# Optimization experiments

Measured on AMD Instinct MI355X. Metric: run time of the kernel, lower is better.

The kernel has to match this reference:

```python
import math
import jax, jax.numpy as jnp
import numpy as np

B = 8
S = 1024  # equal per-sequence length -> cu_seqlens = arange(B+1)*S
H = 16
D = 64


def setup_inputs() -> dict:
    key = jax.random.key(0)
    kq, kk, kv = jax.random.split(key, 3)
    T = B * S
    q = jax.random.normal(kq, (T, H, D), dtype=jnp.float32)
    k = jax.random.normal(kk, (T, H, D), dtype=jnp.float32)
    v = jax.random.normal(kv, (T, H, D), dtype=jnp.float32)
    cu_seqlens = (jnp.arange(B + 1, dtype=jnp.int32) * S)
    return {"q": q, "k": k, "v": v, "cu_seqlens": cu_seqlens, "max_seqlen": S}


def reference(q, k, v, cu_seqlens, max_seqlen):
    # Non-causal varlen attention over packed sequences.
    # q, k, v: [total_tokens, H, D]; cu_seqlens: [B+1] int32.
    # Sequences here are equal-length, so the packed layout reshapes to [B,S,H,D];
    # a cu_seqlens-derived validity mask keeps the math identical to the varlen kernel.
    T, h, d = q.shape
    b = cu_seqlens.shape[0] - 1
    s = T // b
    scale = 1.0 / math.sqrt(d)

    seq_lens = cu_seqlens[1:] - cu_seqlens[:-1]            # [b]
    valid = jnp.arange(s)[None, :] < seq_lens[:, None]      # [b, s] bool

    qb = q.reshape(b, s, h, d)
    kb = k.reshape(b, s, h, d)
    vb = v.reshape(b, s, h, d)

    scores = jnp.einsum("bqhd,bkhd->bhqk", qb, kb) * scale  # [b,h,s,s]
    neg = jnp.asarray(-1e30, dtype=scores.dtype)
    scores = jnp.where(valid[:, None, None, :], scores, neg)
    p = jax.nn.softmax(scores, axis=-1)
    out = jnp.einsum("bhqk,bkhd->bqhd", p, vb)              # [b,s,h,d]
    out = jnp.where(valid[:, :, None, None], out, 0.0)
    return out.reshape(T, h, d)
```

## Files before the change

### kernel.cpp

```cpp
#include <hip/hip_runtime.h>

#define H_DIM 16
#define D_DIM 64
#define QBLK 256
#define KVBLK 64
#define NTHREADS 512
#define TOKSTRIDE (H_DIM * D_DIM)

typedef __bf16 bf16x8 __attribute__((ext_vector_type(8)));
typedef float  f32x4  __attribute__((ext_vector_type(4)));

__global__ __launch_bounds__(NTHREADS, 4)
void attn_fwd(const float* __restrict__ qg, const float* __restrict__ kg,
              const float* __restrict__ vg, const int* __restrict__ cu,
              float* __restrict__ out, int tiles)
{
    __shared__ __align__(16) __bf16 Klds[2][KVBLK * D_DIM];
    __shared__ __align__(16) __bf16 Vlds[2][KVBLK * D_DIM];

    int nwg = gridDim.x;
    int bid = blockIdx.x;
    int lg = ((nwg & 7) == 0) ? ((bid & 7) * (nwg >> 3) + (bid >> 3)) : bid;

    int qt  = lg % tiles;
    int sh  = lg / tiles;
    int h   = sh % H_DIM;
    int seq = sh / H_DIM;

    int cu0 = cu[seq], cu1 = cu[seq + 1];
    int len = cu1 - cu0;
    int q0  = qt * QBLK;
    if (len <= 0 || q0 >= len) return;

    int tid  = threadIdx.x;
    int wid  = tid >> 6;
    int lane = tid & 63;
    int g    = lane >> 4;
    int c    = lane & 15;

    const float SC = 0.125f * 1.44269504088896340736f;

    bf16x8 qf[2][2];
    #pragma unroll
    for (int rg = 0; rg < 2; ++rg) {
        int qrow = q0 + wid * 32 + rg * 16 + c;
        bool valid = qrow < len;
        const float* qp = qg + ((cu0 + qrow) * TOKSTRIDE + h * D_DIM);
        #pragma unroll
        for (int ks = 0; ks < 2; ++ks) {
            float4 a = valid ? *(const float4*)(qp + ks * 32 + g * 8)     : make_float4(0,0,0,0);
            float4 b = valid ? *(const float4*)(qp + ks * 32 + g * 8 + 4) : make_float4(0,0,0,0);
            qf[rg][ks][0] = (__bf16)(a.x * SC); qf[rg][ks][1] = (__bf16)(a.y * SC);
            qf[rg][ks][2] = (__bf16)(a.z * SC); qf[rg][ks][3] = (__bf16)(a.w * SC);
            qf[rg][ks][4] = (__bf16)(b.x * SC); qf[rg][ks][5] = (__bf16)(b.y * SC);
            qf[rg][ks][6] = (__bf16)(b.z * SC); qf[rg][ks][7] = (__bf16)(b.w * SC);
        }
    }

    f32x4 o0[4] = {}, o1[4] = {};
    float m0 = -3.0e38f, m1 = -3.0e38f;
    float l0 = 0.0f,     l1 = 0.0f;

    int krow = tid >> 3;
    int kc   = tid & 7;
    int kwoff = krow * 128 + ((kc * 16) ^ ((krow & 7) << 4));
    int vfg  = tid >> 6;
    int vd   = tid & 63;
    int vr0  = 32 * (vfg >> 2) + 4 * (vfg & 3);

    const float* kptr = kg + (cu0 + krow) * TOKSTRIDE + h * D_DIM + kc * 8;
    const float* vptr = vg + (cu0 + vr0)  * TOKSTRIDE + h * D_DIM + vd;

    float4 ka, kb;
    float  vv[8];

    auto load_fast = [&]() {
        ka = *(const float4*)kptr;
        kb = *(const float4*)(kptr + 4);
        #pragma unroll
        for (int i = 0; i < 8; ++i)
            vv[i] = vptr[(i >> 2) * (16 * TOKSTRIDE) + (i & 3) * TOKSTRIDE];
        kptr += KVBLK * TOKSTRIDE;
        vptr += KVBLK * TOKSTRIDE;
    };
    auto load_tail = [&](int kb0) {
        if (kb0 + krow < len) {
            ka = *(const float4*)kptr;
            kb = *(const float4*)(kptr + 4);
        } else {
            ka = make_float4(0,0,0,0); kb = make_float4(0,0,0,0);
        }
        #pragma unroll
        for (int i = 0; i < 8; ++i) {
            int r = kb0 + vr0 + 16 * (i >> 2) + (i & 3);
            vv[i] = (r < len) ? vptr[(i >> 2) * (16 * TOKSTRIDE) + (i & 3) * TOKSTRIDE] : 0.f;
        }
        kptr += KVBLK * TOKSTRIDE;
        vptr += KVBLK * TOKSTRIDE;
    };
    auto write_tile = [&](int buf) {
        bf16x8 kw;
        kw[0]=(__bf16)ka.x; kw[1]=(__bf16)ka.y; kw[2]=(__bf16)ka.z; kw[3]=(__bf16)ka.w;
        kw[4]=(__bf16)kb.x; kw[5]=(__bf16)kb.y; kw[6]=(__bf16)kb.z; kw[7]=(__bf16)kb.w;
        *(bf16x8*)((char*)Klds[buf] + kwoff) = kw;
        bf16x8 vw;
        #pragma unroll
        for (int i = 0; i < 8; ++i) vw[i] = (__bf16)vv[i];
        *(bf16x8*)(Vlds[buf] + (tid << 3)) = vw;
    };

    int nkv = (len + KVBLK - 1) / KVBLK;

    if (KVBLK <= len) load_fast(); else load_tail(0);
    write_tile(0);
    __syncthreads();

    int cur = 0;
    for (int kt = 0; kt < nkv; ++kt) {
        int kbase = kt * KVBLK;
        bool more = kt + 1 < nkv;
        if (more) {
            int nb0 = kbase + KVBLK;
            if (nb0 + KVBLK <= len) load_fast(); else load_tail(nb0);
        }

        const __bf16* K = Klds[cur];
        f32x4 s0[4] = {}, s1[4] = {};
        __builtin_amdgcn_s_setprio(1);
        #pragma unroll
        for (int b = 0; b < 4; ++b) {
            int rowk = 16 * b + c;
            int swz = (rowk & 7) << 4;
            const char* base = (const char*)K + rowk * 128;
            bf16x8 a0 = *(const bf16x8*)(base + ((16 * g)      ^ swz));
            bf16x8 a1 = *(const bf16x8*)(base + ((64 + 16 * g) ^ swz));
            s0[b] = __builtin_amdgcn_mfma_f32_16x16x32_bf16(a0, qf[0][0], s0[b], 0, 0, 0);
            s0[b] = __builtin_amdgcn_mfma_f32_16x16x32_bf16(a1, qf[0][1], s0[b], 0, 0, 0);
            s1[b] = __builtin_amdgcn_mfma_f32_16x16x32_bf16(a0, qf[1][0], s1[b], 0, 0, 0);
            s1[b] = __builtin_amdgcn_mfma_f32_16x16x32_bf16(a1, qf[1][1], s1[b], 0, 0, 0);
        }
        __builtin_amdgcn_s_setprio(0);

        if (kbase + KVBLK > len) {
            #pragma unroll
            for (int b = 0; b < 4; ++b)
                #pragma unroll
                for (int r = 0; r < 4; ++r)
                    if (kbase + 16 * b + 4 * g + r >= len) { s0[b][r] = -3.0e38f; s1[b][r] = -3.0e38f; }
        }

        float t0 = fmaxf(fmaxf(fmaxf(s0[0][0],s0[0][1]),fmaxf(s0[0][2],s0[0][3])),
                         fmaxf(fmaxf(s0[1][0],s0[1][1]),fmaxf(s0[1][2],s0[1][3])));
        t0 = fmaxf(t0, fmaxf(fmaxf(fmaxf(s0[2][0],s0[2][1]),fmaxf(s0[2][2],s0[2][3])),
                             fmaxf(fmaxf(s0[3][0],s0[3][1]),fmaxf(s0[3][2],s0[3][3]))));
        float t1 = fmaxf(fmaxf(fmaxf(s1[0][0],s1[0][1]),fmaxf(s1[0][2],s1[0][3])),
                         fmaxf(fmaxf(s1[1][0],s1[1][1]),fmaxf(s1[1][2],s1[1][3])));
        t1 = fmaxf(t1, fmaxf(fmaxf(fmaxf(s1[2][0],s1[2][1]),fmaxf(s1[2][2],s1[2][3])),
                             fmaxf(fmaxf(s1[3][0],s1[3][1]),fmaxf(s1[3][2],s1[3][3]))));
        t0 = fmaxf(t0, __shfl_xor(t0, 16));
        t0 = fmaxf(t0, __shfl_xor(t0, 32));
        t1 = fmaxf(t1, __shfl_xor(t1, 16));
        t1 = fmaxf(t1, __shfl_xor(t1, 32));

        int ok = (t0 <= m0 + 8.f) && (t1 <= m1 + 8.f);
        if (!__all(ok)) {
            float mn0 = fmaxf(m0, t0), mn1 = fmaxf(m1, t1);
            float al0 = __builtin_amdgcn_exp2f(m0 - mn0);
            float al1 = __builtin_amdgcn_exp2f(m1 - mn1);
            m0 = mn0; m1 = mn1; l0 *= al0; l1 *= al1;
            #pragma unroll
            for (int r = 0; r < 4; ++r) {
                float a0f = __shfl(al0, 4 * g + r);
                float a1f = __shfl(al1, 4 * g + r);
                #pragma unroll
                for (int nb = 0; nb < 4; ++nb) { o0[nb][r] *= a0f; o1[nb][r] *= a1f; }
            }
        }

        bf16x8 p0[2], p1[2];
        float ps0 = 0.f, ps1 = 0.f;
        #pragma unroll
        for (int M = 0; M < 2; ++M)
            #pragma unroll
            for (int i = 0; i < 8; ++i) {
                float e0 = __builtin_amdgcn_exp2f(s0[2 * M + (i >> 2)][i & 3] - m0);
                float e1 = __builtin_amdgcn_exp2f(s1[2 * M + (i >> 2)][i & 3] - m1);
                p0[M][i] = (__bf16)e0; p1[M][i] = (__bf16)e1;
                ps0 += e0; ps1 += e1;
            }
        ps0 += __shfl_xor(ps0, 16); ps0 += __shfl_xor(ps0, 32);
        ps1 += __shfl_xor(ps1, 16); ps1 += __shfl_xor(ps1, 32);
        l0 += ps0; l1 += ps1;

        const __bf16* V = Vlds[cur];
        __builtin_amdgcn_s_setprio(1);
        #pragma unroll
        for (int nb = 0; nb < 4; ++nb) {
            #pragma unroll
            for (int M = 0; M < 2; ++M) {
                bf16x8 vf = *(const bf16x8*)(V + ((((M << 2) + g) << 6) + (nb << 4) + c) * 8);
                o0[nb] = __builtin_amdgcn_mfma_f32_16x16x32_bf16(p0[M], vf, o0[nb], 0, 0, 0);
                o1[nb] = __builtin_amdgcn_mfma_f32_16x16x32_bf16(p1[M], vf, o1[nb], 0, 0, 0);
            }
        }
        __builtin_amdgcn_s_setprio(0);

        if (more) write_tile(cur ^ 1);
        __syncthreads();
        cur ^= 1;
    }

    #pragma unroll
    for (int r = 0; r < 4; ++r) {
        float lr0 = __shfl(l0, 4 * g + r);
        float lr1 = __shfl(l1, 4 * g + r);
        float li0 = (lr0 > 0.f) ? 1.0f / lr0 : 0.f;
        float li1 = (lr1 > 0.f) ? 1.0f / lr1 : 0.f;
        int qrowA = q0 + wid * 32 + 4 * g + r;
        int qrowB = qrowA + 16;
        if (qrowA < len) {
            float* op = out + ((cu0 + qrowA) * TOKSTRIDE + h * D_DIM);
            #pragma unroll
            for (int nb = 0; nb < 4; ++nb) op[nb * 16 + c] = o0[nb][r] * li0;
        }
        if (qrowB < len) {
            float* op = out + ((cu0 + qrowB) * TOKSTRIDE + h * D_DIM);
            #pragma unroll
            for (int nb = 0; nb < 4; ++nb) op[nb * 16 + c] = o1[nb][r] * li1;
        }
    }
}

extern "C" void kernel_launch(void* const* d_in, const int* in_sizes, int n_in,
                              void* d_out, int out_size, void* d_ws, size_t ws_size,
                              hipStream_t stream) {
    const float* q  = (const float*)d_in[0];
    const float* k  = (const float*)d_in[1];
    const float* v  = (const float*)d_in[2];
    const int*   cu = (const int*)d_in[3];

    int nseq  = in_sizes[3] - 1;
    int T     = in_sizes[0] / (H_DIM * D_DIM);
    int S     = T / nseq;
    int tiles = (S + QBLK - 1) / QBLK;
    int nwg   = nseq * H_DIM * tiles;

    attn_fwd<<<nwg, NTHREADS, 0, stream>>>(q, k, v, cu, (float*)d_out, tiles);
}
```

Before: 61.26 us.

## Compute softmax row sums via MFMA with ones vector and rotate KV start

Replaces the per-lane exp sum and cross-lane shuffle reduction of the softmax denominator with extra MFMAs that multiply the bf16 probabilities by a ones column, so the row sum accumulates in the matrix unit. Half of the workgroups start their KV loop at the middle tile and wrap around, which spreads KV memory traffic across different addresses at the same moment. The row max now uses three-input max chains. The trade-offs: four extra MFMAs per tile, and a denominator summed from bf16-rounded probabilities rather than fp32 values.

```diff
diff --git a/kernel.cpp b/kernel.cpp
--- a/kernel.cpp
+++ b/kernel.cpp
@@ -9,6 +9,8 @@
 
 typedef __bf16 bf16x8 __attribute__((ext_vector_type(8)));
 typedef float  f32x4  __attribute__((ext_vector_type(4)));
+
+#define MAX3(a,b,c) fmaxf(fmaxf((a),(b)),(c))
 
 __global__ __launch_bounds__(NTHREADS, 4)
 void attn_fwd(const float* __restrict__ qg, const float* __restrict__ kg,
@@ -57,9 +59,13 @@
         }
     }
 
+    bf16x8 ones;
+    #pragma unroll
+    for (int i = 0; i < 8; ++i) ones[i] = (c == 0) ? (__bf16)1.0f : (__bf16)0.0f;
+
     f32x4 o0[4] = {}, o1[4] = {};
+    f32x4 o0x = {}, o1x = {};
     float m0 = -3.0e38f, m1 = -3.0e38f;
-    float l0 = 0.0f,     l1 = 0.0f;
 
     int krow = tid >> 3;
     int kc   = tid & 7;
@@ -68,32 +74,34 @@
     int vd   = tid & 63;
     int vr0  = 32 * (vfg >> 2) + 4 * (vfg & 3);
 
-    const float* kptr = kg + (cu0 + krow) * TOKSTRIDE + h * D_DIM + kc * 8;
-    const float* vptr = vg + (cu0 + vr0)  * TOKSTRIDE + h * D_DIM + vd;
+    const float* kbase_ptr = kg + (cu0 + krow) * TOKSTRIDE + h * D_DIM + kc * 8;
+    const float* vbase_ptr = vg + (cu0 + vr0)  * TOKSTRIDE + h * D_DIM + vd;
+    const float* kptr;
+    const float* vptr;
 
     float4 ka, kb;
     float  vv[8];
 
-    auto load_fast = [&]() {
-        ka = *(const float4*)kptr;
-        kb = *(const float4*)(kptr + 4);
-        #pragma unroll
-        for (int i = 0; i < 8; ++i)
-            vv[i] = vptr[(i >> 2) * (16 * TOKSTRIDE) + (i & 3) * TOKSTRIDE];
-        kptr += KVBLK * TOKSTRIDE;
-        vptr += KVBLK * TOKSTRIDE;
-    };
-    auto load_tail = [&](int kb0) {
-        if (kb0 + krow < len) {
+    auto do_load = [&](int kt) {
+        int kb0 = kt * KVBLK;
+        if (kb0 + KVBLK <= len) {
             ka = *(const float4*)kptr;
             kb = *(const float4*)(kptr + 4);
+            #pragma unroll
+            for (int i = 0; i < 8; ++i)
+                vv[i] = vptr[(i >> 2) * (16 * TOKSTRIDE) + (i & 3) * TOKSTRIDE];
         } else {
-            ka = make_float4(0,0,0,0); kb = make_float4(0,0,0,0);
-        }
-        #pragma unroll
-        for (int i = 0; i < 8; ++i) {
-            int r = kb0 + vr0 + 16 * (i >> 2) + (i & 3);
-            vv[i] = (r < len) ? vptr[(i >> 2) * (16 * TOKSTRIDE) + (i & 3) * TOKSTRIDE] : 0.f;
+            if (kb0 + krow < len) {
+                ka = *(const float4*)kptr;
+                kb = *(const float4*)(kptr + 4);
+            } else {
+                ka = make_float4(0,0,0,0); kb = make_float4(0,0,0,0);
+            }
+            #pragma unroll
+            for (int i = 0; i < 8; ++i) {
+                int r = kb0 + vr0 + 16 * (i >> 2) + (i & 3);
+                vv[i] = (r < len) ? vptr[(i >> 2) * (16 * TOKSTRIDE) + (i & 3) * TOKSTRIDE] : 0.f;
+            }
         }
         kptr += KVBLK * TOKSTRIDE;
         vptr += KVBLK * TOKSTRIDE;
@@ -110,18 +118,23 @@
     };
 
     int nkv = (len + KVBLK - 1) / KVBLK;
-
-    if (KVBLK <= len) load_fast(); else load_tail(0);
+    int kt0 = ((2 * bid >= nwg) && nkv > 1) ? (nkv >> 1) : 0;
+
+    kptr = kbase_ptr + (size_t)kt0 * KVBLK * TOKSTRIDE;
+    vptr = vbase_ptr + (size_t)kt0 * KVBLK * TOKSTRIDE;
+    do_load(kt0);
     write_tile(0);
     __syncthreads();
 
     int cur = 0;
-    for (int kt = 0; kt < nkv; ++kt) {
+    int kt = kt0;
+    for (int ii = 0; ii < nkv; ++ii) {
         int kbase = kt * KVBLK;
-        bool more = kt + 1 < nkv;
+        int ktn = (kt + 1 == nkv) ? 0 : kt + 1;
+        bool more = (ii + 1 < nkv);
         if (more) {
-            int nb0 = kbase + KVBLK;
-            if (nb0 + KVBLK <= len) load_fast(); else load_tail(nb0);
+            if (ktn == 0) { kptr = kbase_ptr; vptr = vbase_ptr; }
+            do_load(ktn);
         }
 
         const __bf16* K = Klds[cur];
@@ -149,14 +162,18 @@
                     if (kbase + 16 * b + 4 * g + r >= len) { s0[b][r] = -3.0e38f; s1[b][r] = -3.0e38f; }
         }
 
-        float t0 = fmaxf(fmaxf(fmaxf(s0[0][0],s0[0][1]),fmaxf(s0[0][2],s0[0][3])),
-                         fmaxf(fmaxf(s0[1][0],s0[1][1]),fmaxf(s0[1][2],s0[1][3])));
-        t0 = fmaxf(t0, fmaxf(fmaxf(fmaxf(s0[2][0],s0[2][1]),fmaxf(s0[2][2],s0[2][3])),
-                             fmaxf(fmaxf(s0[3][0],s0[3][1]),fmaxf(s0[3][2],s0[3][3]))));
-        float t1 = fmaxf(fmaxf(fmaxf(s1[0][0],s1[0][1]),fmaxf(s1[0][2],s1[0][3])),
-                         fmaxf(fmaxf(s1[1][0],s1[1][1]),fmaxf(s1[1][2],s1[1][3])));
-        t1 = fmaxf(t1, fmaxf(fmaxf(fmaxf(s1[2][0],s1[2][1]),fmaxf(s1[2][2],s1[2][3])),
-                             fmaxf(fmaxf(s1[3][0],s1[3][1]),fmaxf(s1[3][2],s1[3][3]))));
+        float x0 = MAX3(s0[0][0], s0[0][1], s0[0][2]);
+        float x1 = MAX3(s0[0][3], s0[1][0], s0[1][1]);
+        float x2 = MAX3(s0[1][2], s0[1][3], s0[2][0]);
+        float x3 = MAX3(s0[2][1], s0[2][2], s0[2][3]);
+        float x4 = MAX3(s0[3][0], s0[3][1], s0[3][2]);
+        float t0 = MAX3(MAX3(x0, x1, x2), fmaxf(x3, x4), s0[3][3]);
+        float y0 = MAX3(s1[0][0], s1[0][1], s1[0][2]);
+        float y1 = MAX3(s1[0][3], s1[1][0], s1[1][1]);
+        float y2 = MAX3(s1[1][2], s1[1][3], s1[2][0]);
+        float y3 = MAX3(s1[2][1], s1[2][2], s1[2][3]);
+        float y4 = MAX3(s1[3][0], s1[3][1], s1[3][2]);
+        float t1 = MAX3(MAX3(y0, y1, y2), fmaxf(y3, y4), s1[3][3]);
         t0 = fmaxf(t0, __shfl_xor(t0, 16));
         t0 = fmaxf(t0, __shfl_xor(t0, 32));
         t1 = fmaxf(t1, __shfl_xor(t1, 16));
@@ -167,30 +184,25 @@
             float mn0 = fmaxf(m0, t0), mn1 = fmaxf(m1, t1);
             float al0 = __builtin_amdgcn_exp2f(m0 - mn0);
             float al1 = __builtin_amdgcn_exp2f(m1 - mn1);
-            m0 = mn0; m1 = mn1; l0 *= al0; l1 *= al1;
+            m0 = mn0; m1 = mn1;
             #pragma unroll
             for (int r = 0; r < 4; ++r) {
                 float a0f = __shfl(al0, 4 * g + r);
                 float a1f = __shfl(al1, 4 * g + r);
                 #pragma unroll
                 for (int nb = 0; nb < 4; ++nb) { o0[nb][r] *= a0f; o1[nb][r] *= a1f; }
+                o0x[r] *= a0f; o1x[r] *= a1f;
             }
         }
 
         bf16x8 p0[2], p1[2];
-        float ps0 = 0.f, ps1 = 0.f;
         #pragma unroll
         for (int M = 0; M < 2; ++M)
             #pragma unroll
             for (int i = 0; i < 8; ++i) {
-                float e0 = __builtin_amdgcn_exp2f(s0[2 * M + (i >> 2)][i & 3] - m0);
-                float e1 = __builtin_amdgcn_exp2f(s1[2 * M + (i >> 2)][i & 3] - m1);
-                p0[M][i] = (__bf16)e0; p1[M][i] = (__bf16)e1;
-                ps0 += e0; ps1 += e1;
-            }
-        ps0 += __shfl_xor(ps0, 16); ps0 += __shfl_xor(ps0, 32);
-        ps1 += __shfl_xor(ps1, 16); ps1 += __shfl_xor(ps1, 32);
-        l0 += ps0; l1 += ps1;
+                p0[M][i] = (__bf16)__builtin_amdgcn_exp2f(s0[2 * M + (i >> 2)][i & 3] - m0);
+                p1[M][i] = (__bf16)__builtin_amdgcn_exp2f(s1[2 * M + (i >> 2)][i & 3] - m1);
+            }
 
         const __bf16* V = Vlds[cur];
         __builtin_amdgcn_s_setprio(1);
@@ -203,17 +215,22 @@
                 o1[nb] = __builtin_amdgcn_mfma_f32_16x16x32_bf16(p1[M], vf, o1[nb], 0, 0, 0);
             }
         }
+        o0x = __builtin_amdgcn_mfma_f32_16x16x32_bf16(p0[0], ones, o0x, 0, 0, 0);
+        o0x = __builtin_amdgcn_mfma_f32_16x16x32_bf16(p0[1], ones, o0x, 0, 0, 0);
+        o1x = __builtin_amdgcn_mfma_f32_16x16x32_bf16(p1[0], ones, o1x, 0, 0, 0);
+        o1x = __builtin_amdgcn_mfma_f32_16x16x32_bf16(p1[1], ones, o1x, 0, 0, 0);
         __builtin_amdgcn_s_setprio(0);
 
         if (more) write_tile(cur ^ 1);
         __syncthreads();
         cur ^= 1;
+        kt = ktn;
     }
 
     #pragma unroll
     for (int r = 0; r < 4; ++r) {
-        float lr0 = __shfl(l0, 4 * g + r);
-        float lr1 = __shfl(l1, 4 * g + r);
+        float lr0 = __shfl(o0x[r], 16 * g);
+        float lr1 = __shfl(o1x[r], 16 * g);
         float li0 = (lr0 > 0.f) ? 1.0f / lr0 : 0.f;
         float li1 = (lr1 > 0.f) ? 1.0f / lr1 : 0.f;
         int qrowA = q0 + wid * 32 + 4 * g + r;
```

New measurement: 82.24 us. 34.2% more time.

## Process two KV tiles per barrier using four-slot LDS ring

Applied to the files above, without the earlier changes.

Grows the K/V LDS buffers from two to four slots and restructures the main loop so each iteration computes two KV tiles before a single __syncthreads, halving the number of block-wide barriers. The load and write logic is merged into one helper and the per-tile compute is factored into a lambda. Doubling LDS to 32 KB per block may limit how many blocks fit per CU under the launch bounds of 4, and it adds register pressure from the duplicated inlined compute.

```diff
diff --git a/kernel.cpp b/kernel.cpp
--- a/kernel.cpp
+++ b/kernel.cpp
@@ -15,8 +15,8 @@
               const float* __restrict__ vg, const int* __restrict__ cu,
               float* __restrict__ out, int tiles)
 {
-    __shared__ __align__(16) __bf16 Klds[2][KVBLK * D_DIM];
-    __shared__ __align__(16) __bf16 Vlds[2][KVBLK * D_DIM];
+    __shared__ __align__(16) __bf16 Klds[4][KVBLK * D_DIM];
+    __shared__ __align__(16) __bf16 Vlds[4][KVBLK * D_DIM];
 
     int nwg = gridDim.x;
     int bid = blockIdx.x;
@@ -74,26 +74,25 @@
     float4 ka, kb;
     float  vv[8];
 
-    auto load_fast = [&]() {
-        ka = *(const float4*)kptr;
-        kb = *(const float4*)(kptr + 4);
-        #pragma unroll
-        for (int i = 0; i < 8; ++i)
-            vv[i] = vptr[(i >> 2) * (16 * TOKSTRIDE) + (i & 3) * TOKSTRIDE];
-        kptr += KVBLK * TOKSTRIDE;
-        vptr += KVBLK * TOKSTRIDE;
-    };
-    auto load_tail = [&](int kb0) {
-        if (kb0 + krow < len) {
+    auto do_load = [&](int kb0) {
+        if (kb0 + KVBLK <= len) {
             ka = *(const float4*)kptr;
             kb = *(const float4*)(kptr + 4);
+            #pragma unroll
+            for (int i = 0; i < 8; ++i)
+                vv[i] = vptr[(i >> 2) * (16 * TOKSTRIDE) + (i & 3) * TOKSTRIDE];
         } else {
-            ka = make_float4(0,0,0,0); kb = make_float4(0,0,0,0);
-        }
-        #pragma unroll
-        for (int i = 0; i < 8; ++i) {
-            int r = kb0 + vr0 + 16 * (i >> 2) + (i & 3);
-            vv[i] = (r < len) ? vptr[(i >> 2) * (16 * TOKSTRIDE) + (i & 3) * TOKSTRIDE] : 0.f;
+            if (kb0 + krow < len) {
+                ka = *(const float4*)kptr;
+                kb = *(const float4*)(kptr + 4);
+            } else {
+                ka = make_float4(0,0,0,0); kb = make_float4(0,0,0,0);
+            }
+            #pragma unroll
+            for (int i = 0; i < 8; ++i) {
+                int r = kb0 + vr0 + 16 * (i >> 2) + (i & 3);
+                vv[i] = (r < len) ? vptr[(i >> 2) * (16 * TOKSTRIDE) + (i & 3) * TOKSTRIDE] : 0.f;
+            }
         }
         kptr += KVBLK * TOKSTRIDE;
         vptr += KVBLK * TOKSTRIDE;
@@ -109,22 +108,8 @@
         *(bf16x8*)(Vlds[buf] + (tid << 3)) = vw;
     };
 
-    int nkv = (len + KVBLK - 1) / KVBLK;
-
-    if (KVBLK <= len) load_fast(); else load_tail(0);
-    write_tile(0);
-    __syncthreads();
-
-    int cur = 0;
-    for (int kt = 0; kt < nkv; ++kt) {
-        int kbase = kt * KVBLK;
-        bool more = kt + 1 < nkv;
-        if (more) {
-            int nb0 = kbase + KVBLK;
-            if (nb0 + KVBLK <= len) load_fast(); else load_tail(nb0);
-        }
-
-        const __bf16* K = Klds[cur];
+    auto compute_tile = [&](int buf, int kbase) {
+        const __bf16* K = Klds[buf];
         f32x4 s0[4] = {}, s1[4] = {};
         __builtin_amdgcn_s_setprio(1);
         #pragma unroll
@@ -149,14 +134,16 @@
                     if (kbase + 16 * b + 4 * g + r >= len) { s0[b][r] = -3.0e38f; s1[b][r] = -3.0e38f; }
         }
 
-        float t0 = fmaxf(fmaxf(fmaxf(s0[0][0],s0[0][1]),fmaxf(s0[0][2],s0[0][3])),
-                         fmaxf(fmaxf(s0[1][0],s0[1][1]),fmaxf(s0[1][2],s0[1][3])));
-        t0 = fmaxf(t0, fmaxf(fmaxf(fmaxf(s0[2][0],s0[2][1]),fmaxf(s0[2][2],s0[2][3])),
-                             fmaxf(fmaxf(s0[3][0],s0[3][1]),fmaxf(s0[3][2],s0[3][3]))));
-        float t1 = fmaxf(fmaxf(fmaxf(s1[0][0],s1[0][1]),fmaxf(s1[0][2],s1[0][3])),
-                         fmaxf(fmaxf(s1[1][0],s1[1][1]),fmaxf(s1[1][2],s1[1][3])));
-        t1 = fmaxf(t1, fmaxf(fmaxf(fmaxf(s1[2][0],s1[2][1]),fmaxf(s1[2][2],s1[2][3])),
-                             fmaxf(fmaxf(s1[3][0],s1[3][1]),fmaxf(s1[3][2],s1[3][3]))));
+        float b0 = fmaxf(fmaxf(s0[0][0], s0[0][1]), fmaxf(s0[0][2], s0[0][3]));
+        float b1 = fmaxf(fmaxf(s0[1][0], s0[1][1]), fmaxf(s0[1][2], s0[1][3]));
+        float b2 = fmaxf(fmaxf(s0[2][0], s0[2][1]), fmaxf(s0[2][2], s0[2][3]));
+        float b3 = fmaxf(fmaxf(s0[3][0], s0[3][1]), fmaxf(s0[3][2], s0[3][3]));
+        float t0 = fmaxf(fmaxf(b0, b1), fmaxf(b2, b3));
+        float y0 = fmaxf(fmaxf(s1[0][0], s1[0][1]), fmaxf(s1[0][2], s1[0][3]));
+        float y1 = fmaxf(fmaxf(s1[1][0], s1[1][1]), fmaxf(s1[1][2], s1[1][3]));
+        float y2 = fmaxf(fmaxf(s1[2][0], s1[2][1]), fmaxf(s1[2][2], s1[2][3]));
+        float y3 = fmaxf(fmaxf(s1[3][0], s1[3][1]), fmaxf(s1[3][2], s1[3][3]));
+        float t1 = fmaxf(fmaxf(y0, y1), fmaxf(y2, y3));
         t0 = fmaxf(t0, __shfl_xor(t0, 16));
         t0 = fmaxf(t0, __shfl_xor(t0, 32));
         t1 = fmaxf(t1, __shfl_xor(t1, 16));
@@ -192,7 +179,7 @@
         ps1 += __shfl_xor(ps1, 16); ps1 += __shfl_xor(ps1, 32);
         l0 += ps0; l1 += ps1;
 
-        const __bf16* V = Vlds[cur];
+        const __bf16* V = Vlds[buf];
         __builtin_amdgcn_s_setprio(1);
         #pragma unroll
         for (int nb = 0; nb < 4; ++nb) {
@@ -204,10 +191,31 @@
             }
         }
         __builtin_amdgcn_s_setprio(0);
-
-        if (more) write_tile(cur ^ 1);
+    };
+
+    int nkv = (len + KVBLK - 1) / KVBLK;
+
+    do_load(0);
+    write_tile(0);
+    if (nkv > 1) { do_load(KVBLK); write_tile(1); }
+    __syncthreads();
+
+    for (int kt = 0; kt < nkv; kt += 2) {
+        int pb = (kt >> 1) & 1;
+        int nb = pb ^ 1;
+        bool moreA = kt + 2 < nkv;
+        bool moreB = kt + 3 < nkv;
+
+        if (moreA) do_load((kt + 2) * KVBLK);
+        compute_tile(pb * 2, kt * KVBLK);
+        if (moreA) write_tile(nb * 2);
+
+        if (kt + 1 < nkv) {
+            if (moreB) do_load((kt + 3) * KVBLK);
+            compute_tile(pb * 2 + 1, (kt + 1) * KVBLK);
+            if (moreB) write_tile(nb * 2 + 1);
+        }
         __syncthreads();
-        cur ^= 1;
     }
 
     #pragma unroll
```

Result: slower. 63.39 us (+3.5%).
